# Performance work log

Hardware: AMD Instinct MI355X
Metric: run time of the kernel (lower is better)

## Reference

```python
import jax, jax.numpy as jnp
import numpy as np
from jax import lax

VOCAB, E, HD = 50000, 128, 256
H = HD // 2            # per-direction LSTM hidden
K = 9                  # tagset size
START, STOP = 7, 8
B, T = 64, 1024
NEG = -10000.0


def setup_inputs() -> dict:
    key = jax.random.key(0)
    ks = jax.random.split(key, 14)
    s = 0.1
    sentence = jax.random.randint(ks[0], (B, T), 0, VOCAB)
    embed = jax.random.normal(ks[1], (VOCAB, E), jnp.float32) * s
    w_ih_f = jax.random.normal(ks[2], (4 * H, E), jnp.float32) * s
    w_hh_f = jax.random.normal(ks[3], (4 * H, H), jnp.float32) * s
    b_ih_f = jax.random.normal(ks[4], (4 * H,), jnp.float32) * s
    b_hh_f = jax.random.normal(ks[5], (4 * H,), jnp.float32) * s
    w_ih_b = jax.random.normal(ks[6], (4 * H, E), jnp.float32) * s
    w_hh_b = jax.random.normal(ks[7], (4 * H, H), jnp.float32) * s
    b_ih_b = jax.random.normal(ks[8], (4 * H,), jnp.float32) * s
    b_hh_b = jax.random.normal(ks[9], (4 * H,), jnp.float32) * s
    w_out = jax.random.normal(ks[10], (K, HD), jnp.float32) * s
    b_out = jax.random.normal(ks[11], (K,), jnp.float32) * s
    transitions = jax.random.normal(ks[12], (K, K), jnp.float32)
    transitions = transitions.at[START, :].set(NEG).at[:, STOP].set(NEG)
    return dict(sentence=sentence, embed=embed,
                w_ih_f=w_ih_f, w_hh_f=w_hh_f, b_ih_f=b_ih_f, b_hh_f=b_hh_f,
                w_ih_b=w_ih_b, w_hh_b=w_hh_b, b_ih_b=b_ih_b, b_hh_b=b_hh_b,
                w_out=w_out, b_out=b_out, transitions=transitions)


def _lstm_dir(x_tbe, w_ih, w_hh, b_ih, b_hh):
    # x_tbe: [T, B, E] -> hidden states [T, B, H]; zero initial state
    # (original passes no hidden to self.lstm, so PyTorch uses zeros)
    bsz = x_tbe.shape[1]
    def step(carry, x_t):
        h, c = carry
        gates = x_t @ w_ih.T + b_ih + h @ w_hh.T + b_hh   # [B, 4H]
        i, f, g, o = jnp.split(gates, 4, axis=-1)          # torch gate order
        i, f, o = jax.nn.sigmoid(i), jax.nn.sigmoid(f), jax.nn.sigmoid(o)
        g = jnp.tanh(g)
        c = f * c + i * g
        h = o * jnp.tanh(c)
        return (h, c), h
    init = (jnp.zeros((bsz, H), x_tbe.dtype), jnp.zeros((bsz, H), x_tbe.dtype))
    _, hs = lax.scan(step, init, x_tbe)
    return hs


def _features(sentence, embed, w_ih_f, w_hh_f, b_ih_f, b_hh_f,
              w_ih_b, w_hh_b, b_ih_b, b_hh_b, w_out, b_out):
    x = embed[sentence]                      # [B, T, E]
    x_tbe = jnp.transpose(x, (1, 0, 2))      # [T, B, E]
    h_f = _lstm_dir(x_tbe, w_ih_f, w_hh_f, b_ih_f, b_hh_f)
    h_b = _lstm_dir(x_tbe[::-1], w_ih_b, w_hh_b, b_ih_b, b_hh_b)[::-1]
    h = jnp.concatenate([h_f, h_b], axis=-1)  # [T, B, 2H]
    feats = h @ w_out.T + b_out               # [T, B, K]
    return feats


def _viterbi(feats_tbk, transitions):
    # feats_tbk: [T, B, K]. Batched version of _viterbi_decode.
    bsz = feats_tbk.shape[1]
    init = jnp.full((K,), NEG, feats_tbk.dtype).at[START].set(0.0)
    delta0 = jnp.broadcast_to(init, (bsz, K))
    def step(delta, feat_t):
        # scores[b, next, prev] = delta[b, prev] + trans[next, prev]
        scores = delta[:, None, :] + transitions[None, :, :]
        bp = jnp.argmax(scores, axis=-1)                 # [B, K]
        delta = jnp.max(scores, axis=-1) + feat_t        # [B, K]
        return delta, bp
    delta, bps = lax.scan(step, delta0, feats_tbk)       # bps: [T, B, K]
    terminal = delta + transitions[STOP][None, :]
    best_last = jnp.argmax(terminal, axis=-1)            # [B]
    score = jnp.max(terminal, axis=-1)                   # [B]
    def back(tag, bp_t):
        prev = jnp.take_along_axis(bp_t, tag[:, None], axis=1)[:, 0]
        return prev, prev
    _, path_rev = lax.scan(back, best_last, bps[::-1])   # [T, B]
    # path_rev reversed = [START, tag_0, ..., tag_{T-2}] -> drop START, add last
    path = jnp.concatenate([path_rev[::-1][1:], best_last[None, :]], axis=0)
    return score, jnp.transpose(path, (1, 0))            # [B], [B, T]


def reference(sentence, embed, w_ih_f, w_hh_f, b_ih_f, b_hh_f,
              w_ih_b, w_hh_b, b_ih_b, b_hh_b, w_out, b_out, transitions):
    feats = _features(sentence, embed, w_ih_f, w_hh_f, b_ih_f, b_hh_f,
                      w_ih_b, w_hh_b, b_ih_b, b_hh_b, w_out, b_out)
    score, tag_seq = _viterbi(feats, transitions)
    return score, tag_seq
```

## Files before the change

kernel.cpp:

```cpp
#include <hip/hip_runtime.h>
#include <hip/hip_bf16.h>

#define Tn 1024
#define Bn 64
#define En 128
#define G4 512
#define NEGV -10000.0f

typedef short bh8 __attribute__((ext_vector_type(8)));
typedef float fl4 __attribute__((ext_vector_type(4)));
typedef int i8v __attribute__((ext_vector_type(8)));

#if __has_builtin(__builtin_amdgcn_exp2f)
#define EXP2(x) __builtin_amdgcn_exp2f(x)
#else
#define EXP2(x) exp2f(x)
#endif
#if __has_builtin(__builtin_amdgcn_rcpf)
#define RCP(x) __builtin_amdgcn_rcpf(x)
#else
#define RCP(x) (1.0f / (x))
#endif

#define LOG2E  1.4426950408889634f
#define LOG2E2 2.8853900817779268f

__device__ __forceinline__ float bf2f(unsigned short u) {
    unsigned int v = ((unsigned int)u) << 16;
    float f;
    __builtin_memcpy(&f, &v, 4);
    return f;
}
__device__ __forceinline__ unsigned short f2bf(float f) {
    unsigned int u;
    __builtin_memcpy(&u, &f, 4);
    u = (u + 0x7fffu + ((u >> 16) & 1u)) >> 16;
    return (unsigned short)u;
}
__device__ __forceinline__ unsigned cvt_pk_bf16(float lo, float hi) {
    unsigned r;
    asm("v_cvt_pk_bf16_f32 %0, %1, %2" : "=v"(r) : "v"(lo), "v"(hi));
    return r;
}
__device__ __forceinline__ unsigned short f2bf_hw(float x) {
    return (unsigned short)(cvt_pk_bf16(x, 0.0f) & 0xffffu);
}
__device__ __forceinline__ float asf(unsigned int u) {
    float f;
    __builtin_memcpy(&f, &u, 4);
    return f;
}
__device__ __forceinline__ float i2f(int u) {
    float f;
    __builtin_memcpy(&f, &u, 4);
    return f;
}
__device__ __forceinline__ int f2i(float f) {
    int u;
    __builtin_memcpy(&u, &f, 4);
    return u;
}

__device__ __forceinline__ unsigned char f8enc(float x) {
#if __has_builtin(__builtin_amdgcn_cvt_pk_fp8_f32)
    int pk = __builtin_amdgcn_cvt_pk_fp8_f32(x, 0.0f, 0, false);
    return (unsigned char)(pk & 0xff);
#else
    unsigned u;
    __builtin_memcpy(&u, &x, 4);
    unsigned s = (u >> 31) << 7;
    float a = fabsf(x);
    if (!(a > 0.0f)) return (unsigned char)s;
    if (a >= 464.0f) return (unsigned char)(s | 0x7E);
    if (a < 0.015625f) {
        int q = (int)rintf(a * 512.0f);
        return (unsigned char)(s | (unsigned)q);
    }
    int ex;
    (void)frexpf(a, &ex);
    int E = ex - 1;
    float t = ldexpf(a, -E);
    int m3 = (int)rintf((t - 1.0f) * 8.0f);
    if (m3 == 8) { m3 = 0; E += 1; }
    if (E > 8) return (unsigned char)(s | 0x7E);
    return (unsigned char)(s | ((unsigned)(E + 7) << 3) | (unsigned)m3);
#endif
}

__device__ __forceinline__ void barrier_lds_only() {
    __builtin_amdgcn_s_waitcnt(0xC07F);
    __builtin_amdgcn_s_barrier();
}

__global__ __launch_bounds__(256) void k_wcvt(
    const float* __restrict__ wf, const float* __restrict__ wb,
    const float* __restrict__ wih_f, const float* __restrict__ wih_b,
    unsigned char* __restrict__ o, unsigned short* __restrict__ wihP)
{
    const int i = blockIdx.x * 256 + threadIdx.x;
    if (i < 131072) {
        const float v = (i < 65536) ? wf[i] : wb[i - 65536];
        o[i] = f8enc(v * 64.0f);
    } else {
        const int j = i - 131072;
        const int dir = j >> 16;
        const int np = (j >> 7) & 511;
        const int k = j & 127;
        const int norig = ((np & 3) << 7) + (np >> 2);
        const float* w = dir ? wih_b : wih_f;
        wihP[j] = f2bf_hw(w[norig * 128 + k]);
    }
}

__global__ __launch_bounds__(256) void k_inproj(
    const int* __restrict__ sent, const float* __restrict__ embed,
    const unsigned short* __restrict__ wihP,
    const float* __restrict__ b_ih_f, const float* __restrict__ b_hh_f,
    const float* __restrict__ b_ih_b, const float* __restrict__ b_hh_b,
    unsigned short* __restrict__ G_f, unsigned short* __restrict__ G_b)
{
    __shared__ unsigned short Asm[128][136];
    __shared__ unsigned short Bsm[2][128][136];
    const int tid = threadIdx.x;
    const int mt = blockIdx.x;
    const int r0 = mt * 128;

    {
        const int srow = tid >> 1;
        const int ch = (tid & 1) * 64;
        const int rg = r0 + srow;
        const int tt = rg >> 6, bb = rg & 63;
        const int tok = sent[bb * Tn + tt];
        const float* ar = embed + (size_t)tok * En + ch;
#pragma unroll
        for (int i = 0; i < 64; i += 4) {
            float4 v = *(const float4*)(ar + i);
            *(unsigned*)&Asm[srow][ch + i]     = cvt_pk_bf16(v.x, v.y);
            *(unsigned*)&Asm[srow][ch + i + 2] = cvt_pk_bf16(v.z, v.w);
        }
    }

    const int brow = tid >> 1;
    const int bhalf = (tid & 1) * 64;
#define STAGE_B(cidx)                                                          \
    {                                                                          \
        const int d_ = (cidx) >> 2, nt_ = (cidx) & 3, pb_ = (cidx) & 1;        \
        const uint4* s4 = (const uint4*)(wihP + ((size_t)d_ << 16) +           \
                          (size_t)(nt_ * 128 + brow) * 128 + bhalf);           \
        uint4* d4 = (uint4*)&Bsm[pb_][brow][bhalf];                            \
        _Pragma("unroll")                                                      \
        for (int ii = 0; ii < 8; ++ii) d4[ii] = s4[ii];                        \
    }

    STAGE_B(0);
    __syncthreads();

    const int w = tid >> 6, lane = tid & 63;
    const int ln = lane & 15, lq = lane >> 4;
    const int nwb = w * 32;

    for (int cidx = 0; cidx < 8; ++cidx) {
        if (cidx + 1 < 8) STAGE_B(cidx + 1);
        const int dir = cidx >> 2, nt = cidx & 3, pb = cidx & 1;

        fl4 acc[8][2];
#pragma unroll
        for (int mi = 0; mi < 8; ++mi)
#pragma unroll
            for (int ni = 0; ni < 2; ++ni) acc[mi][ni] = (fl4){0.f, 0.f, 0.f, 0.f};

#pragma unroll
        for (int kt = 0; kt < 4; ++kt) {
            const int kc = kt * 32 + lq * 8;
            bh8 a[8], bf[2];
#pragma unroll
            for (int mi = 0; mi < 8; ++mi) a[mi] = *(const bh8*)&Asm[mi * 16 + ln][kc];
#pragma unroll
            for (int ni = 0; ni < 2; ++ni) bf[ni] = *(const bh8*)&Bsm[pb][nwb + ni * 16 + ln][kc];
#pragma unroll
            for (int mi = 0; mi < 8; ++mi)
#pragma unroll
                for (int ni = 0; ni < 2; ++ni)
                    acc[mi][ni] = __builtin_amdgcn_mfma_f32_16x16x32_bf16(a[mi], bf[ni], acc[mi][ni], 0, 0, 0);
        }

        const float* bi = dir ? b_ih_b : b_ih_f;
        const float* bh = dir ? b_hh_b : b_hh_f;
        unsigned short* Gout = dir ? G_b : G_f;

        float bias[2], gsc[2];
#pragma unroll
        for (int ni = 0; ni < 2; ++ni) {
            const int np = nt * 128 + nwb + ni * 16 + ln;
            const int norig = ((np & 3) << 7) + (np >> 2);
            bias[ni] = bi[norig] + bh[norig];
            gsc[ni] = ((np & 3) == 2) ? LOG2E2 : LOG2E;
        }
#pragma unroll
        for (int mi = 0; mi < 8; ++mi)
#pragma unroll
            for (int ni = 0; ni < 2; ++ni) {
                const int np = nt * 128 + nwb + ni * 16 + ln;
#pragma unroll
                for (int rg = 0; rg < 4; ++rg) {
                    const int m = mi * 16 + lq * 4 + rg;
                    const size_t r = (size_t)(r0 + m);
                    Gout[(r << 9) + np] = f2bf_hw((acc[mi][ni][rg] + bias[ni]) * gsc[ni]);
                }
            }

        __syncthreads();
    }
#undef STAGE_B
}

__global__ __launch_bounds__(512, 2) void k_lstm(
    const unsigned char* __restrict__ whh8,
    const unsigned short* __restrict__ G_f, const unsigned short* __restrict__ G_b,
    unsigned short* __restrict__ h_f, unsigned short* __restrict__ h_b)
{
    const int tid = threadIdx.x;
    const int w = tid >> 6;
    const int lane = tid & 63;
    const int ln = lane & 15;
    const int quad = lane >> 4;
    const int b = blockIdx.x;
    const int dir = blockIdx.y;
    const unsigned short* Gd = dir ? G_b : G_f;
    unsigned short* ho = dir ? h_b : h_f;

    const int j = w * 16 + ln;

    __shared__ __align__(16) unsigned char hls8[2][128];

    const unsigned char* wb8 = whh8 + (size_t)dir * 65536 + quad * 32;
    const i8v w0 = *(const i8v*)(wb8 + ((size_t)(0 * 128 + j) << 7));
    const i8v w1 = *(const i8v*)(wb8 + ((size_t)(1 * 128 + j) << 7));
    const i8v w2 = *(const i8v*)(wb8 + ((size_t)(2 * 128 + j) << 7));
    const i8v w3 = *(const i8v*)(wb8 + ((size_t)(3 * 128 + j) << 7));

    if (tid < 64) ((unsigned*)hls8)[tid] = 0u;
    float c = 0.0f;
    __syncthreads();

    uint2 gp[4];
#pragma unroll
    for (int u = 0; u < 4; ++u) {
        const int tt = dir ? (Tn - 1 - u) : u;
        gp[u] = *(const uint2*)(Gd + (((size_t)tt * Bn + b) << 9) + (j << 2));
    }

    const float dsL  = 0.0009765625f * LOG2E;
    const float ds2L = 0.0009765625f * LOG2E2;

    const float cds = (quad == 2) ? ds2L : -dsL;
    const unsigned gsign = (quad == 2) ? 0u : 0x80000000u;
    const int gshift = (quad & 1) ? 0 : 16;
    const int bp0 = (0 * 16 + ln) << 2;
    const int bp1 = (1 * 16 + ln) << 2;
    const int bp2 = (2 * 16 + ln) << 2;
    const int bp3 = (3 * 16 + ln) << 2;

    for (int blk = 0; blk < Tn / 4; ++blk) {
#pragma unroll
        for (int u = 0; u < 4; ++u) {
            const int s = blk * 4 + u;
            const int t = dir ? (Tn - 1 - s) : s;
            const int p = u & 1;

            const uint2 gv = gp[u];

            if (s + 4 < Tn) {
                const int tt = dir ? (Tn - 5 - s) : (s + 4);
                gp[u] = *(const uint2*)(Gd + (((size_t)tt * Bn + b) << 9) + (j << 2));
            }

            const i8v ha = *(const i8v*)&hls8[p][quad * 32];

            const fl4 z = (fl4){0.f, 0.f, 0.f, 0.f};
            fl4 a0 = __builtin_amdgcn_mfma_scale_f32_16x16x128_f8f6f4(
                         ha, w0, z, 0, 0, 0, 0x7F7F7F7F, 0, 0x7F7F7F7F);
            fl4 a1 = __builtin_amdgcn_mfma_scale_f32_16x16x128_f8f6f4(
                         ha, w1, z, 0, 0, 0, 0x7F7F7F7F, 0, 0x7F7F7F7F);
            fl4 a2 = __builtin_amdgcn_mfma_scale_f32_16x16x128_f8f6f4(
                         ha, w2, z, 0, 0, 0, 0x7F7F7F7F, 0, 0x7F7F7F7F);
            fl4 a3 = __builtin_amdgcn_mfma_scale_f32_16x16x128_f8f6f4(
                         ha, w3, z, 0, 0, 0, 0x7F7F7F7F, 0, 0x7F7F7F7F);

            float a01 = (quad & 1) ? a1[0] : a0[0];
            float a23 = (quad & 1) ? a3[0] : a2[0];
            float aown = (quad & 2) ? a23 : a01;
            unsigned wsel = (quad & 2) ? gv.y : gv.x;
            unsigned gb = ((wsel << gshift) & 0xffff0000u) ^ gsign;
            float pre = __builtin_fmaf(aown, cds, asf(gb));
            float tq = RCP(1.0f + EXP2(pre));
            int tqi = f2i(tq);
            float iv = i2f(__builtin_amdgcn_ds_bpermute(bp0, tqi));
            float fv = i2f(__builtin_amdgcn_ds_bpermute(bp1, tqi));
            float tg = i2f(__builtin_amdgcn_ds_bpermute(bp2, tqi));
            float ov = i2f(__builtin_amdgcn_ds_bpermute(bp3, tqi));
            float gvv = __builtin_fmaf(-2.0f, tg, 1.0f);
            c = __builtin_fmaf(fv, c, iv * gvv);
            float r2 = RCP(1.0f + EXP2(c * LOG2E2));
            float hn = ov * __builtin_fmaf(-2.0f, r2, 1.0f);

            if (quad == 0) {
                hls8[1 - p][j] = f8enc(hn * 16.0f);
                ho[(((size_t)t * Bn + b) << 7) + j] = f2bf(hn);
            }

            barrier_lds_only();
        }
    }
}

__global__ __launch_bounds__(256) void k_feats(
    const unsigned short* __restrict__ h_f, const unsigned short* __restrict__ h_b,
    const float* __restrict__ w_out, const float* __restrict__ b_out,
    float* __restrict__ feats)
{
    __shared__ float wl[256][12];
    __shared__ float bl[12];
    const int tid = threadIdx.x;
#pragma unroll
    for (int s = 0; s < 9; ++s) wl[tid][s] = w_out[s * 256 + tid];
#pragma unroll
    for (int s = 9; s < 12; ++s) wl[tid][s] = 0.0f;
    if (tid < 12) bl[tid] = (tid < 9) ? b_out[tid] : 0.0f;
    __syncthreads();

    const int r = blockIdx.x * 256 + tid;
    const unsigned short* hfr = h_f + (size_t)r * 128;
    const unsigned short* hbr = h_b + (size_t)r * 128;
    float acc[12];
#pragma unroll
    for (int k = 0; k < 12; ++k) acc[k] = bl[k];

    for (int ch = 0; ch < 32; ++ch) {
        const unsigned short* src = (ch < 16) ? (hfr + ch * 8) : (hbr + (ch - 16) * 8);
        uint4 hv = *(const uint4*)src;
        unsigned int hw0 = hv.x, hw1 = hv.y, hw2 = hv.z, hw3 = hv.w;
        const int jb = ch * 8;
#pragma unroll
        for (int q = 0; q < 8; ++q) {
            unsigned int word = (q < 2) ? hw0 : ((q < 4) ? hw1 : ((q < 6) ? hw2 : hw3));
            unsigned short hs = (q & 1) ? (unsigned short)(word >> 16) : (unsigned short)(word & 0xffff);
            float hf = bf2f(hs);
            const float* wrp = &wl[jb + q][0];
            float4 w0 = *(const float4*)(wrp);
            float4 w1 = *(const float4*)(wrp + 4);
            float4 w2 = *(const float4*)(wrp + 8);
            acc[0] += hf * w0.x; acc[1] += hf * w0.y; acc[2] += hf * w0.z; acc[3] += hf * w0.w;
            acc[4] += hf * w1.x; acc[5] += hf * w1.y; acc[6] += hf * w1.z; acc[7] += hf * w1.w;
            acc[8] += hf * w2.x; acc[9] += hf * w2.y; acc[10] += hf * w2.z; acc[11] += hf * w2.w;
        }
    }
    const int t = r >> 6, b = r & 63;
    float* fr = feats + (size_t)b * 9216 + (size_t)t * 9;
#pragma unroll
    for (int k = 0; k < 9; ++k) fr[k] = acc[k];
}

__global__ __launch_bounds__(64) void k_viterbi(
    const float* __restrict__ feats, const float* __restrict__ trans,
    float* __restrict__ out)
{
    __shared__ __align__(16) unsigned char bp[1024 * 16];
    __shared__ __align__(16) float fl[1024 * 9];
    __shared__ unsigned char pt[1024];

    const int b = blockIdx.x, tid = threadIdx.x;

    {
        const float4* fsrc = (const float4*)(feats + (size_t)b * 9216);
        float4* fdst = (float4*)fl;
        for (int i = tid; i < 2304; i += 64) fdst[i] = fsrc[i];
    }

    const int n9 = (tid < 9) ? tid : 8;
    float trn[9];
#pragma unroll
    for (int p = 0; p < 9; ++p) trn[p] = trans[n9 * 9 + p];
    float trs = (tid < 9) ? trans[8 * 9 + tid] : -3.0e38f;

    float delta = (n9 == 7) ? 0.0f : NEGV;
    __syncthreads();

    float fnext = fl[n9];
    for (int t = 0; t < 1024; ++t) {
        float d0 = __shfl(delta, 0, 64);
        float d1 = __shfl(delta, 1, 64);
        float d2 = __shfl(delta, 2, 64);
        float d3 = __shfl(delta, 3, 64);
        float d4 = __shfl(delta, 4, 64);
        float d5 = __shfl(delta, 5, 64);
        float d6 = __shfl(delta, 6, 64);
        float d7 = __shfl(delta, 7, 64);
        float d8 = __shfl(delta, 8, 64);
        float fhere = fnext;
        if (t < 1023) fnext = fl[(t + 1) * 9 + n9];

        float s0 = d0 + trn[0], s1 = d1 + trn[1], s2 = d2 + trn[2];
        float s3 = d3 + trn[3], s4 = d4 + trn[4], s5 = d5 + trn[5];
        float s6 = d6 + trn[6], s7 = d7 + trn[7], s8 = d8 + trn[8];

        float m012 = fmaxf(fmaxf(s0, s1), s2);
        float m345 = fmaxf(fmaxf(s3, s4), s5);
        float m678 = fmaxf(fmaxf(s6, s7), s8);
        float m = fmaxf(fmaxf(m012, m345), m678);
        delta = m + fhere;

        float v01 = (s1 > s0) ? s1 : s0; int a01 = (s1 > s0) ? 1 : 0;
        float v23 = (s3 > s2) ? s3 : s2; int a23 = (s3 > s2) ? 3 : 2;
        float v45 = (s5 > s4) ? s5 : s4; int a45 = (s5 > s4) ? 5 : 4;
        float v67 = (s7 > s6) ? s7 : s6; int a67 = (s7 > s6) ? 7 : 6;
        float v03 = (v23 > v01) ? v23 : v01; int a03 = (v23 > v01) ? a23 : a01;
        float v47 = (v67 > v45) ? v67 : v45; int a47 = (v67 > v45) ? a67 : a45;
        float v07 = (v47 > v03) ? v47 : v03; int a07 = (v47 > v03) ? a47 : a03;
        int am = (s8 > v07) ? 8 : a07;

        if (tid < 9) bp[t * 16 + tid] = (unsigned char)am;
    }

    float tv = (tid < 9) ? (delta + trs) : -3.0e38f;
    int bi = tid;
#pragma unroll
    for (int off = 8; off >= 1; off >>= 1) {
        float ov = __shfl_down(tv, off, 64);
        int oi = __shfl_down(bi, off, 64);
        if (ov > tv || (ov == tv && oi < bi)) { tv = ov; bi = oi; }
    }
    int best = __shfl(bi, 0, 64);
    if (tid == 0) out[b] = tv;

    if (tid == 0) {
        int tag = best;
        for (int t0 = 1023; t0 >= 0; t0 -= 8) {
            uint4 rows[8];
#pragma unroll
            for (int i = 0; i < 8; ++i) rows[i] = *(const uint4*)&bp[(t0 - i) * 16];
#pragma unroll
            for (int i = 0; i < 8; ++i) {
                pt[t0 - i] = (unsigned char)tag;
                uint4 rw = rows[i];
                unsigned int sel = (unsigned int)tag >> 2;
                unsigned int word = (sel == 0) ? rw.x : ((sel == 1) ? rw.y : rw.z);
                tag = (int)((word >> ((tag & 3) * 8)) & 0xffu);
            }
        }
    }
    for (int i = tid; i < 1024; i += 64) {
        out[64 + b * 1024 + i] = (float)pt[i];
    }
}

extern "C" void kernel_launch(void* const* d_in, const int* in_sizes, int n_in,
                              void* d_out, int out_size, void* d_ws, size_t ws_size,
                              hipStream_t stream) {
    const int*   sent   = (const int*)d_in[0];
    const float* embed  = (const float*)d_in[1];
    const float* w_ih_f = (const float*)d_in[2];
    const float* w_hh_f = (const float*)d_in[3];
    const float* b_ih_f = (const float*)d_in[4];
    const float* b_hh_f = (const float*)d_in[5];
    const float* w_ih_b = (const float*)d_in[6];
    const float* w_hh_b = (const float*)d_in[7];
    const float* b_ih_b = (const float*)d_in[8];
    const float* b_hh_b = (const float*)d_in[9];
    const float* w_out  = (const float*)d_in[10];
    const float* b_out  = (const float*)d_in[11];
    const float* trans  = (const float*)d_in[12];
    float* out = (float*)d_out;

    unsigned short* G_f = (unsigned short*)d_ws;
    unsigned short* G_b = G_f + (size_t)Tn * Bn * G4;
    unsigned short* h_f = G_b + (size_t)Tn * Bn * G4;
    unsigned short* h_b = h_f + (size_t)Tn * Bn * 128;
    float* feats = (float*)(h_b + (size_t)Tn * Bn * 128);
    unsigned char* whh8 = (unsigned char*)(feats + (size_t)Tn * Bn * 9);
    unsigned short* wihP = (unsigned short*)(whh8 + 131072);

    k_wcvt<<<1024, 256, 0, stream>>>(w_hh_f, w_hh_b, w_ih_f, w_ih_b, whh8, wihP);
    k_inproj<<<512, 256, 0, stream>>>(sent, embed, wihP,
        b_ih_f, b_hh_f, b_ih_b, b_hh_b, G_f, G_b);
    k_lstm<<<dim3(64, 2), 512, 0, stream>>>(whh8, G_f, G_b, h_f, h_b);
    k_feats<<<256, 256, 0, stream>>>(h_f, h_b, w_out, b_out, feats);
    k_viterbi<<<64, 64, 0, stream>>>(feats, trans, out);
}
```

Baseline: 737.8 us.

## Fuse LSTM directions into one block and replace barriers with LDS counter spin-waits

Both LSTM directions now run in a single 1024-thread workgroup per batch row instead of two 512-thread blocks. The per-step workgroup barrier is replaced by a per-direction LDS atomic counter that each wave increments and polls, with a 4-slot ring buffer for the FP8 hidden state. The goal is to let waves of each direction proceed without a full barrier and to decouple the two chains. The trade-offs are that only 64 CUs are used, both directions share one CU's MFMA and LDS, and spin polling adds LDS traffic. The iteration-budget escape could silently break synchronization.

```diff
diff --git a/kernel.cpp b/kernel.cpp
--- a/kernel.cpp
+++ b/kernel.cpp
@@ -85,11 +85,6 @@
     if (E > 8) return (unsigned char)(s | 0x7E);
     return (unsigned char)(s | ((unsigned)(E + 7) << 3) | (unsigned)m3);
 #endif
-}
-
-__device__ __forceinline__ void barrier_lds_only() {
-    __builtin_amdgcn_s_waitcnt(0xC07F);
-    __builtin_amdgcn_s_barrier();
 }
 
 __global__ __launch_bounds__(256) void k_wcvt(
@@ -214,24 +209,26 @@
 #undef STAGE_B
 }
 
-__global__ __launch_bounds__(512, 2) void k_lstm(
+__global__ __launch_bounds__(1024, 1) void k_lstm(
     const unsigned char* __restrict__ whh8,
     const unsigned short* __restrict__ G_f, const unsigned short* __restrict__ G_b,
     unsigned short* __restrict__ h_f, unsigned short* __restrict__ h_b)
 {
     const int tid = threadIdx.x;
-    const int w = tid >> 6;
+    const int chain = tid >> 9;
+    const int w = (tid >> 6) & 7;
     const int lane = tid & 63;
     const int ln = lane & 15;
     const int quad = lane >> 4;
     const int b = blockIdx.x;
-    const int dir = blockIdx.y;
+    const int dir = chain;
     const unsigned short* Gd = dir ? G_b : G_f;
     unsigned short* ho = dir ? h_b : h_f;
 
     const int j = w * 16 + ln;
 
-    __shared__ __align__(16) unsigned char hls8[2][128];
+    __shared__ __align__(16) unsigned char hls8[2][4][128];
+    __shared__ unsigned scnt[2][32];
 
     const unsigned char* wb8 = whh8 + (size_t)dir * 65536 + quad * 32;
     const i8v w0 = *(const i8v*)(wb8 + ((size_t)(0 * 128 + j) << 7));
@@ -239,7 +236,8 @@
     const i8v w2 = *(const i8v*)(wb8 + ((size_t)(2 * 128 + j) << 7));
     const i8v w3 = *(const i8v*)(wb8 + ((size_t)(3 * 128 + j) << 7));
 
-    if (tid < 64) ((unsigned*)hls8)[tid] = 0u;
+    if (tid < 256) ((unsigned*)hls8)[tid] = 0u;
+    if (tid < 2) scnt[tid][0] = 0u;
     float c = 0.0f;
     __syncthreads();
 
@@ -261,12 +259,13 @@
     const int bp2 = (2 * 16 + ln) << 2;
     const int bp3 = (3 * 16 + ln) << 2;
 
+    int budget = 1 << 24;
+
     for (int blk = 0; blk < Tn / 4; ++blk) {
 #pragma unroll
         for (int u = 0; u < 4; ++u) {
             const int s = blk * 4 + u;
             const int t = dir ? (Tn - 1 - s) : s;
-            const int p = u & 1;
 
             const uint2 gv = gp[u];
 
@@ -275,7 +274,15 @@
                 gp[u] = *(const uint2*)(Gd + (((size_t)tt * Bn + b) << 9) + (j << 2));
             }
 
-            const i8v ha = *(const i8v*)&hls8[p][quad * 32];
+            if (s > 0) {
+                const unsigned tgt = (unsigned)s * 8u;
+                while (__hip_atomic_load(&scnt[chain][0], __ATOMIC_ACQUIRE,
+                                         __HIP_MEMORY_SCOPE_WORKGROUP) < tgt) {
+                    if (--budget <= 0) break;
+                }
+            }
+
+            const i8v ha = *(const i8v*)&hls8[chain][(u + 3) & 3][quad * 32];
 
             const fl4 z = (fl4){0.f, 0.f, 0.f, 0.f};
             fl4 a0 = __builtin_amdgcn_mfma_scale_f32_16x16x128_f8f6f4(
@@ -305,11 +312,13 @@
             float hn = ov * __builtin_fmaf(-2.0f, r2, 1.0f);
 
             if (quad == 0) {
-                hls8[1 - p][j] = f8enc(hn * 16.0f);
+                hls8[chain][u][j] = f8enc(hn * 16.0f);
                 ho[(((size_t)t * Bn + b) << 7) + j] = f2bf(hn);
             }
 
-            barrier_lds_only();
+            if (lane == 0)
+                __hip_atomic_fetch_add(&scnt[chain][0], 1u, __ATOMIC_RELEASE,
+                                       __HIP_MEMORY_SCOPE_WORKGROUP);
         }
     }
 }
@@ -483,7 +492,7 @@
     k_wcvt<<<1024, 256, 0, stream>>>(w_hh_f, w_hh_b, w_ih_f, w_ih_b, whh8, wihP);
     k_inproj<<<512, 256, 0, stream>>>(sent, embed, wihP,
         b_ih_f, b_hh_f, b_ih_b, b_hh_b, G_f, G_b);
-    k_lstm<<<dim3(64, 2), 512, 0, stream>>>(whh8, G_f, G_b, h_f, h_b);
+    k_lstm<<<dim3(64), 1024, 0, stream>>>(whh8, G_f, G_b, h_f, h_b);
     k_feats<<<256, 256, 0, stream>>>(h_f, h_b, w_out, b_out, feats);
     k_viterbi<<<64, 64, 0, stream>>>(feats, trans, out);
 }
```

After: 994.0 us. 34.7% more time.
